# Kernel tuning notes

Measured on AMD Instinct MI355X. Metric: run time of the kernel, lower is better.

## Reference

```python
import jax, jax.numpy as jnp
import numpy as np
import math

D_MODEL = 1024
NHEAD = 16
HEAD_DIM = D_MODEL // NHEAD
ROPE_BASE = 10000.0


def _rope(x):
    # x: [B, H, S, Dh]; rotate per the RoPE class (half-split variant)
    d = x.shape[-1]
    half = d // 2
    seq_len = x.shape[2]
    theta = 1.0 / (ROPE_BASE ** (jnp.arange(0, d, 2, dtype=jnp.float32) / d))  # [d/2]
    ang = jnp.arange(seq_len, dtype=jnp.float32)[:, None] * theta[None, :]      # [S, d/2]
    ang2 = jnp.concatenate([ang, ang], axis=-1)                                 # [S, d]
    cos_ = jnp.cos(ang2)[None, None, :, :]
    sin_ = jnp.sin(ang2)[None, None, :, :]
    neg_half = jnp.concatenate([-x[..., half:], x[..., :half]], axis=-1)
    return x * cos_ + neg_half * sin_


def setup_inputs() -> dict:
    key = jax.random.key(0)
    ks = jax.random.split(key, 10)
    B, S, D = 4, 2048, D_MODEL
    scale = 1.0 / math.sqrt(D)
    x = jax.random.normal(ks[0], (B, S, D), dtype=jnp.float32)
    Wq = jax.random.normal(ks[1], (D, D), dtype=jnp.float32) * scale
    bq = jnp.zeros((D,), dtype=jnp.float32)
    Wk = jax.random.normal(ks[2], (D, D), dtype=jnp.float32) * scale
    bk = jnp.zeros((D,), dtype=jnp.float32)
    Wv = jax.random.normal(ks[3], (D, D), dtype=jnp.float32) * scale
    bv = jnp.zeros((D,), dtype=jnp.float32)
    Wo = jax.random.normal(ks[4], (D, D), dtype=jnp.float32) * scale
    bo = jnp.zeros((D,), dtype=jnp.float32)
    # causal mask: mask==1 means masked (upper triangle)
    mask = jnp.triu(jnp.ones((S, S), dtype=jnp.int32), k=1)[None, None, :, :]
    return {"x": x, "Wq": Wq, "bq": bq, "Wk": Wk, "bk": bk,
            "Wv": Wv, "bv": bv, "Wo": Wo, "bo": bo, "mask": mask}


def reference(x, Wq, bq, Wk, bk, Wv, bv, Wo, bo, mask):
    B, S, D = x.shape
    H, Dh = NHEAD, HEAD_DIM

    def proj(W, b):
        y = jnp.einsum('bsd,ed->bse', x, W) + b  # torch Linear: x @ W.T + b
        return y.reshape(B, S, H, Dh).transpose(0, 2, 1, 3)  # [B,H,S,Dh]

    q = _rope(proj(Wq, bq))
    k = _rope(proj(Wk, bk))
    v = proj(Wv, bv)

    a = jnp.einsum('bhqd,bhkd->bhqk', q, k) / math.sqrt(Dh)  # [B,H,S,S]
    a = jnp.where(mask == 1, jnp.float32(-1e9), a)
    a = jax.nn.softmax(a, axis=-1)
    out = jnp.einsum('bhqk,bhkd->bhqd', a, v)                 # [B,H,S,Dh]
    out = out.transpose(0, 2, 1, 3).reshape(B, S, D)
    return jnp.einsum('bsd,ed->bse', out, Wo) + bo
```

## Files before the change

### kernel.cpp

```cpp
#include <hip/hip_runtime.h>
#include <stdint.h>

typedef unsigned short u16;
typedef __bf16 bf16x8 __attribute__((ext_vector_type(8)));
typedef __bf16 bf16x2 __attribute__((ext_vector_type(2)));
typedef float f32x4 __attribute__((ext_vector_type(4)));
typedef float f32x16 __attribute__((ext_vector_type(16)));

#define SEQ    2048
#define NHEAD  16
#define DH     64
#define DMODEL 1024
#define NBH    64

__device__ __forceinline__ u16 cvt1(float f){
  union { __bf16 h; u16 u; } c; c.h = (__bf16)f; return c.u;
}
__device__ __forceinline__ uint32_t cvt2(float a, float b){
  union { bf16x2 v; uint32_t u; } c; c.v = bf16x2{(__bf16)a, (__bf16)b}; return c.u;
}
__device__ __forceinline__ int swz(int row){ return (((row&7)^((row>>3)&7))<<4); }

#if __has_builtin(__builtin_amdgcn_exp2f)
__device__ __forceinline__ float EXP2(float x){ return __builtin_amdgcn_exp2f(x); }
#else
__device__ __forceinline__ float EXP2(float x){ return exp2f(x); }
#endif
__device__ __forceinline__ float max3f(float a, float b, float c){
  float r; asm("v_max3_f32 %0, %1, %2, %3" : "=v"(r) : "v"(a), "v"(b), "v"(c));
  return r;
}

typedef const __attribute__((address_space(1))) uint32_t* gas_t;
typedef __attribute__((address_space(3))) uint32_t* las_t;
__device__ __forceinline__ void async16(const void* g, void* l){
  __builtin_amdgcn_global_load_lds((gas_t)g, (las_t)l, 16, 0, 0);
}

__device__ __forceinline__ void vstore8(char* dst, uint2 a0, uint2 a1,
                                        uint2 b0, uint2 b1, int dc, int vpos){
  uint32_t pk[8];
  pk[0] = __builtin_amdgcn_perm(b0.x, a0.x, 0x05040100u);
  pk[1] = __builtin_amdgcn_perm(b0.x, a0.x, 0x07060302u);
  pk[2] = __builtin_amdgcn_perm(b0.y, a0.y, 0x05040100u);
  pk[3] = __builtin_amdgcn_perm(b0.y, a0.y, 0x07060302u);
  pk[4] = __builtin_amdgcn_perm(b1.x, a1.x, 0x05040100u);
  pk[5] = __builtin_amdgcn_perm(b1.x, a1.x, 0x07060302u);
  pk[6] = __builtin_amdgcn_perm(b1.y, a1.y, 0x05040100u);
  pk[7] = __builtin_amdgcn_perm(b1.y, a1.y, 0x07060302u);
#pragma unroll
  for (int e=0;e<8;e++){
    const int row = dc*8 + e;
    *(uint32_t*)(dst + ((row*128 + vpos*2) ^ swz(row))) = pk[e];
  }
}

__global__ void prep(const float* __restrict__ x,  const float* __restrict__ Wq,
                     const float* __restrict__ Wk, const float* __restrict__ Wv,
                     const float* __restrict__ Wo,
                     u16* __restrict__ xb, u16* __restrict__ wqkv,
                     u16* __restrict__ wob, float* __restrict__ tab)
{
  const int bid = blockIdx.x, tid = threadIdx.x;
  if (bid < 6144){
    const float* src; u16* dst; int lb;
    if      (bid < 4096){ src = x;  dst = xb;              lb = bid; }
    else if (bid < 4608){ src = Wq; dst = wqkv;            lb = bid-4096; }
    else if (bid < 5120){ src = Wk; dst = wqkv + 1048576;  lb = bid-4608; }
    else if (bid < 5632){ src = Wv; dst = wqkv + 2097152;  lb = bid-5120; }
    else                { src = Wo; dst = wob;             lb = bid-5632; }
    const size_t off = (size_t)lb*2048 + tid*8;
    float4 a = *(const float4*)(src+off);
    float4 b = *(const float4*)(src+off+4);
    bf16x8 o = { (__bf16)a.x,(__bf16)a.y,(__bf16)a.z,(__bf16)a.w,
                 (__bf16)b.x,(__bf16)b.y,(__bf16)b.z,(__bf16)b.w };
    *(bf16x8*)(dst+off) = o;
  } else {
    const int t = (bid-6144)*256 + tid;
    const int s = t >> 5, j = t & 31;
    double freq = exp(-(double)(2*j)/64.0*log(10000.0));
    double ang = (double)s*freq;
    tab[s*64 + 2*j]     = (float)cos(ang);
    tab[s*64 + 2*j + 1] = (float)sin(ang);
  }
}

template<int MODE>
__global__ __launch_bounds__(256, 2)
void gemm_bt(const u16* __restrict__ A, const u16* __restrict__ W,
             const float* __restrict__ b0, const float* __restrict__ b1,
             const float* __restrict__ b2, float* __restrict__ fout,
             u16* __restrict__ dq, u16* __restrict__ dk, u16* __restrict__ dv,
             const float* __restrict__ tab)
{
  __shared__ u16 Ab[2][128*32];
  __shared__ u16 Bb[2][128*32];
  const int tid = threadIdx.x;
  const int lane = tid & 63;
  const int w = tid >> 6, wr = w >> 1, wc = w & 1;
  const int m0 = blockIdx.y * 128;
  const int n0 = blockIdx.x * 128;
  const int c0 = lane & 15, g = lane >> 4;

  f32x4 acc[4][4] = {};

  const int sr = tid >> 2;
  const int sc16 = tid & 3;
  const int stoff = sr*64 + sc16*16;
  const int gsw = (sc16*16) ^ ((sr & 3) << 4);
  const char* ga = (const char*)A + (size_t)(m0 + sr)*DMODEL*2 + gsw;
  const char* gb = (const char*)W + (size_t)(n0 + sr)*DMODEL*2 + gsw;

#define STAGE_G(buf, kk) do{ \
    async16(ga + 2*(kk),              (char*)Ab[buf] + stoff); \
    async16(ga + 2*(kk) + 128*DMODEL, (char*)Ab[buf] + stoff + 4096); \
    async16(gb + 2*(kk),              (char*)Bb[buf] + stoff); \
    async16(gb + 2*(kk) + 128*DMODEL, (char*)Bb[buf] + stoff + 4096); \
  }while(0)

#define COMPUTE_G(buf) do{ \
    bf16x8 afr[4], bfr[4]; \
    _Pragma("unroll") \
    for (int i=0;i<4;i++){ \
      const int row = wr*64 + i*16 + c0; \
      afr[i] = *(const bf16x8*)((const char*)Ab[buf] + row*64 + ((g*16) ^ ((row&3)<<4))); \
    } \
    _Pragma("unroll") \
    for (int j=0;j<4;j++){ \
      const int row = wc*64 + j*16 + c0; \
      bfr[j] = *(const bf16x8*)((const char*)Bb[buf] + row*64 + ((g*16) ^ ((row&3)<<4))); \
    } \
    __builtin_amdgcn_s_setprio(1); \
    _Pragma("unroll") \
    for (int i=0;i<4;i++) \
      _Pragma("unroll") \
      for (int j=0;j<4;j++) \
        acc[i][j] = __builtin_amdgcn_mfma_f32_16x16x32_bf16(afr[i], bfr[j], acc[i][j], 0,0,0); \
    __builtin_amdgcn_s_setprio(0); \
  }while(0)

  STAGE_G(0, 0);
#pragma unroll 2
  for (int k0 = 0; k0 < DMODEL - 32; k0 += 32) {
    const int cur = (k0 >> 5) & 1;
    STAGE_G(cur ^ 1, k0 + 32);
    asm volatile("s_waitcnt vmcnt(4)" ::: "memory");
    __builtin_amdgcn_s_barrier();
    __builtin_amdgcn_sched_barrier(0);
    COMPUTE_G(cur);
    __builtin_amdgcn_s_barrier();
    __builtin_amdgcn_sched_barrier(0);
  }
  asm volatile("s_waitcnt vmcnt(0)" ::: "memory");
  __builtin_amdgcn_s_barrier();
  __builtin_amdgcn_sched_barrier(0);
  COMPUTE_G(1);
#undef STAGE_G
#undef COMPUTE_G

  const int nbase = n0 + wc*64;
  const int t = n0 >> 10;
  const float* bias = (MODE==1) ? b0 : (t==0) ? b0 : (t==1) ? b1 : b2;
  float bv4[4];
#pragma unroll
  for (int j=0;j<4;j++) bv4[j] = bias[(nbase & 1023) + j*16 + c0];

  if (MODE == 0) {
    u16* dst = (t==0) ? dq : (t==1) ? dk : dv;
    const float qs = (t==0) ? 0.18033688011f : 1.0f;
    const int h = (nbase >> 6) & (NHEAD-1);
#pragma unroll
    for (int i=0;i<4;i++){
      const int mbase = m0 + wr*64 + i*16 + g*4;
#pragma unroll
      for (int r=0;r<4;r++){
        const int mm = mbase + r;
        const int bb = mm >> 11, s = mm & (SEQ-1);
        const size_t rowbase = (((size_t)(bb*NHEAD + h))*SEQ + s)*DH;
        if (t < 2) {
#pragma unroll
          for (int j2=0;j2<2;j2++){
            const int dh = j2*16 + c0;
            const float xl = acc[i][j2][r]   + bv4[j2];
            const float xh = acc[i][j2+2][r] + bv4[j2+2];
            const float2 cs = *(const float2*)(tab + (size_t)s*64 + dh*2);
            dst[rowbase + dh]      = cvt1((xl*cs.x - xh*cs.y)*qs);
            dst[rowbase + dh + 32] = cvt1((xh*cs.x + xl*cs.y)*qs);
          }
        } else {
#pragma unroll
          for (int j=0;j<4;j++)
            dst[rowbase + j*16 + c0] = cvt1(acc[i][j][r] + bv4[j]);
        }
      }
    }
  } else {
#pragma unroll
    for (int i=0;i<4;i++){
      const int mbase = m0 + wr*64 + i*16 + g*4;
#pragma unroll
      for (int j=0;j<4;j++){
#pragma unroll
        for (int r=0;r<4;r++)
          fout[(size_t)(mbase + r) * DMODEL + nbase + j*16 + c0] = acc[i][j][r] + bv4[j];
      }
    }
  }
}

__global__ __launch_bounds__(256, 2)
void attn_fwd(const u16* __restrict__ Q, const u16* __restrict__ K,
              const u16* __restrict__ V, u16* __restrict__ O)
{
  __shared__ u16 Kb[2][64*64];
  __shared__ u16 Vt[2][64*64];
  const int bh = blockIdx.x;
  const int pair = blockIdx.y;
  const int tid = threadIdx.x, lane = tid & 63, w = tid >> 6;
  const int c31 = lane & 31, hi = lane >> 5;
  const size_t hb = (size_t)bh * SEQ * DH;
  const int b = bh >> 4, h = bh & 15;

  const int boff1 = tid*16;
  const int ksw1  = boff1 ^ swz(boff1 >> 7);
  const int boff2 = boff1 + 4096;
  const int ksw2  = boff2 ^ swz(boff2 >> 7);
  const int rp = tid >> 3, dc = tid & 7;
  const int kv0 = 2*rp;
  const int vpos = (kv0 & 0x33) | ((kv0 & 4) << 1) | ((kv0 & 8) >> 1);

#pragma unroll 1
  for (int half = 0; half < 2; half++){
    const int qt = half ? (15 - pair) : pair;
    const int qrow_base = qt*128 + w*32;
    const int jt_last  = 2*qt + 1;
    const int jt_end_w = 2*qt + (w>>1);
    const int q = qrow_base + c31;

    bf16x8 qf[4];
#pragma unroll
    for (int kc=0;kc<4;kc++)
      qf[kc] = *(const bf16x8*)(Q + hb + (size_t)q*DH + kc*16 + hi*8);

    f32x16 oacc0 = {}, oacc1 = {};
    float mrun = -3.0e38f, lrun = 0.f;

    {
      const char* gk = (const char*)(K + hb);
      async16(gk + ksw1, (char*)Kb[0] + boff1);
      async16(gk + ksw2, (char*)Kb[0] + boff2);
      const u16* gv = V + hb;
      uint2 a0 = *(const uint2*)(gv + (kv0  )*DH + dc*8);
      uint2 a1 = *(const uint2*)(gv + (kv0  )*DH + dc*8 + 4);
      uint2 b0 = *(const uint2*)(gv + (kv0+1)*DH + dc*8);
      uint2 b1 = *(const uint2*)(gv + (kv0+1)*DH + dc*8 + 4);
      vstore8((char*)Vt[0], a0, a1, b0, b1, dc, vpos);
    }
    __syncthreads();

    uint2 pa0, pa1, pb0, pb1;
    for (int jt = 0; jt <= jt_last; jt++){
      const int cur = jt & 1, nxt = cur ^ 1;
      const bool pre = (jt < jt_last);
      if (pre){
        const char* gk = (const char*)(K + hb + (size_t)(jt+1)*64*DH);
        async16(gk + ksw1, (char*)Kb[nxt] + boff1);
        async16(gk + ksw2, (char*)Kb[nxt] + boff2);
        const u16* gv = V + hb + (size_t)(jt+1)*64*DH;
        pa0 = *(const uint2*)(gv + (kv0  )*DH + dc*8);
        pa1 = *(const uint2*)(gv + (kv0  )*DH + dc*8 + 4);
        pb0 = *(const uint2*)(gv + (kv0+1)*DH + dc*8);
        pb1 = *(const uint2*)(gv + (kv0+1)*DH + dc*8 + 4);
      }

      if (jt <= jt_end_w){
        f32x16 sT[2] = {};
#pragma unroll
        for (int kc=0;kc<4;kc++){
          const int col = (kc*16 + hi*8)*2;
          const int r0 = c31, r1 = 32 + c31;
          const bf16x8 kf0 = *(const bf16x8*)((const char*)Kb[cur] + ((r0*128 + col) ^ swz(r0)));
          const bf16x8 kf1 = *(const bf16x8*)((const char*)Kb[cur] + ((r1*128 + col) ^ swz(r1)));
          __builtin_amdgcn_s_setprio(1);
          sT[0] = __builtin_amdgcn_mfma_f32_32x32x16_bf16(kf0, qf[kc], sT[0], 0,0,0);
          sT[1] = __builtin_amdgcn_mfma_f32_32x32x16_bf16(kf1, qf[kc], sT[1], 0,0,0);
          __builtin_amdgcn_s_setprio(0);
        }
        if (jt == jt_end_w){
#pragma unroll
          for (int kvb=0;kvb<2;kvb++)
#pragma unroll
            for (int r=0;r<16;r++){
              const int kv = jt*64 + kvb*32 + (r&3) + 8*(r>>2) + 4*hi;
              sT[kvb][r] = (kv <= q) ? sT[kvb][r] : -3.0e38f;
            }
        }
        float mx0 = -3.0e38f, mx1 = -3.0e38f;
#pragma unroll
        for (int r=0;r<16;r+=2){
          mx0 = max3f(mx0, sT[0][r], sT[0][r+1]);
          mx1 = max3f(mx1, sT[1][r], sT[1][r+1]);
        }
        float mx = fmaxf(mx0, mx1);
        mx = fmaxf(mx, __shfl_xor(mx, 32));
        const bool grow = __any(mx > mrun + 8.0f);
        float corr = 1.0f;
        if (grow){
          const float mnew = fmaxf(mrun, mx);
          corr = EXP2(mrun - mnew);
          mrun = mnew;
        }
        float ls[4] = {0.f, 0.f, 0.f, 0.f};
#pragma unroll
        for (int kvb=0;kvb<2;kvb++)
#pragma unroll
          for (int r=0;r<16;r++){
            const float p = EXP2(sT[kvb][r] - mrun);
            sT[kvb][r] = p;
            ls[r & 3] += p;
          }
        float lsum = (ls[0] + ls[1]) + (ls[2] + ls[3]);
        lsum += __shfl_xor(lsum, 32);
        lrun = lrun*corr + lsum;
        if (grow){
#pragma unroll
          for (int r=0;r<16;r++){ oacc0[r] *= corr; oacc1[r] *= corr; }
        }
#pragma unroll
        for (int kvb=0;kvb<2;kvb++)
#pragma unroll
          for (int s=0;s<2;s++){
            union { bf16x8 v; uint32_t d[4]; } pa;
#pragma unroll
            for (int j=0;j<4;j++)
              pa.d[j] = cvt2(sT[kvb][s*8+2*j], sT[kvb][s*8+2*j+1]);
            const int col = (kvb*32 + s*16 + hi*8)*2;
            const int r0 = c31, r1 = 32 + c31;
            const bf16x8 vf0 = *(const bf16x8*)((const char*)Vt[cur] + ((r0*128 + col) ^ swz(r0)));
            const bf16x8 vf1 = *(const bf16x8*)((const char*)Vt[cur] + ((r1*128 + col) ^ swz(r1)));
            __builtin_amdgcn_s_setprio(1);
            oacc0 = __builtin_amdgcn_mfma_f32_32x32x16_bf16(vf0, pa.v, oacc0, 0,0,0);
            oacc1 = __builtin_amdgcn_mfma_f32_32x32x16_bf16(vf1, pa.v, oacc1, 0,0,0);
            __builtin_amdgcn_s_setprio(0);
          }
      }

      if (pre) vstore8((char*)Vt[nxt], pa0, pa1, pb0, pb1, dc, vpos);
      __syncthreads();
    }

    {
      const float inv = 1.0f / lrun;
      u16* orow = O + ((size_t)b*SEQ + q)*DMODEL + h*DH;
#pragma unroll
      for (int r2=0;r2<8;r2++){
        const int dh0 = 2*(r2&1) + 8*(r2>>1) + 4*hi;
        *(uint32_t*)(orow + dh0)      = cvt2(oacc0[2*r2]*inv, oacc0[2*r2+1]*inv);
        *(uint32_t*)(orow + 32 + dh0) = cvt2(oacc1[2*r2]*inv, oacc1[2*r2+1]*inv);
      }
    }
  }
}

extern "C" void kernel_launch(void* const* d_in, const int* in_sizes, int n_in,
                              void* d_out, int out_size, void* d_ws, size_t ws_size,
                              hipStream_t stream)
{
  const float* x  = (const float*)d_in[0];
  const float* Wq = (const float*)d_in[1];
  const float* bq = (const float*)d_in[2];
  const float* Wk = (const float*)d_in[3];
  const float* bk = (const float*)d_in[4];
  const float* Wv = (const float*)d_in[5];
  const float* bv = (const float*)d_in[6];
  const float* Wo = (const float*)d_in[7];
  const float* bo = (const float*)d_in[8];

  const size_t MB = 1024*1024;
  char* ws = (char*)d_ws;
  u16*  xb   = (u16*)(ws);
  u16*  aw   = (u16*)(ws);
  u16*  vw   = (u16*)(ws + 16*MB);
  u16*  wqkv = (u16*)(ws + 32*MB);
  u16*  wob  = (u16*)(ws + 38*MB);
  float* tab = (float*)(ws + 41*MB);
  u16*  qw = (u16*)d_out;
  u16*  kw = (u16*)d_out + 8*MB;

  prep<<<dim3(6400), dim3(256), 0, stream>>>(x, Wq, Wk, Wv, Wo, xb, wqkv, wob, tab);

  gemm_bt<0><<<dim3(24, 64), dim3(256), 0, stream>>>(xb, wqkv, bq, bk, bv,
                                                     nullptr, qw, kw, vw, tab);

  attn_fwd<<<dim3(64, 8), dim3(256), 0, stream>>>(qw, kw, vw, aw);

  gemm_bt<1><<<dim3(8, 64), dim3(256), 0, stream>>>(aw, wob, bo, nullptr, nullptr,
                                                    (float*)d_out, nullptr, nullptr, nullptr, nullptr);
}
```

Baseline: 172.2 us.

## Triple-buffer GEMM K-loop and remap block IDs for L2 tile locality

The GEMM's shared-memory staging goes from double to triple buffering, so global loads run two K-steps ahead of compute. The loop is manually unrolled by three, with a deeper vmcnt wait and an explicit two-step tail. The 2D grid becomes a 1D grid with a swizzled block-to-tile mapping that groups M tiles, aiming for better L2 reuse of A/W panels. The extra shared memory (48KB per block) may reduce occupancy relative to the launch_bounds target.

```diff
diff --git a/kernel.cpp b/kernel.cpp
--- a/kernel.cpp
+++ b/kernel.cpp
@@ -93,13 +93,16 @@
              u16* __restrict__ dq, u16* __restrict__ dk, u16* __restrict__ dv,
              const float* __restrict__ tab)
 {
-  __shared__ u16 Ab[2][128*32];
-  __shared__ u16 Bb[2][128*32];
+  __shared__ u16 Ab[3][128*32];
+  __shared__ u16 Bb[3][128*32];
   const int tid = threadIdx.x;
   const int lane = tid & 63;
   const int w = tid >> 6, wr = w >> 1, wc = w & 1;
-  const int m0 = blockIdx.y * 128;
-  const int n0 = blockIdx.x * 128;
+  const int id = blockIdx.x;
+  const int bx = id >> 6;
+  const int by = ((id & 7) << 3) | ((id >> 3) & 7);
+  const int m0 = by * 128;
+  const int n0 = bx * 128;
   const int c0 = lane & 15, g = lane >> 4;
 
   f32x4 acc[4][4] = {};
@@ -139,24 +142,38 @@
     __builtin_amdgcn_s_setprio(0); \
   }while(0)
 
+#define PHASE_G(itv, sb, cb) do{ \
+    STAGE_G(sb, ((itv)+2)*32); \
+    asm volatile("s_waitcnt vmcnt(8)" ::: "memory"); \
+    __builtin_amdgcn_s_barrier(); \
+    __builtin_amdgcn_sched_barrier(0); \
+    COMPUTE_G(cb); \
+    __builtin_amdgcn_s_barrier(); \
+    __builtin_amdgcn_sched_barrier(0); \
+  }while(0)
+
   STAGE_G(0, 0);
-#pragma unroll 2
-  for (int k0 = 0; k0 < DMODEL - 32; k0 += 32) {
-    const int cur = (k0 >> 5) & 1;
-    STAGE_G(cur ^ 1, k0 + 32);
-    asm volatile("s_waitcnt vmcnt(4)" ::: "memory");
-    __builtin_amdgcn_s_barrier();
-    __builtin_amdgcn_sched_barrier(0);
-    COMPUTE_G(cur);
-    __builtin_amdgcn_s_barrier();
-    __builtin_amdgcn_sched_barrier(0);
+  STAGE_G(1, 32);
+#pragma unroll 1
+  for (int j3 = 0; j3 < 10; ++j3) {
+    const int it = 3*j3;
+    PHASE_G(it,   2, 0);
+    PHASE_G(it+1, 0, 1);
+    PHASE_G(it+2, 1, 2);
   }
+  asm volatile("s_waitcnt vmcnt(4)" ::: "memory");
+  __builtin_amdgcn_s_barrier();
+  __builtin_amdgcn_sched_barrier(0);
+  COMPUTE_G(0);
+  __builtin_amdgcn_s_barrier();
+  __builtin_amdgcn_sched_barrier(0);
   asm volatile("s_waitcnt vmcnt(0)" ::: "memory");
   __builtin_amdgcn_s_barrier();
   __builtin_amdgcn_sched_barrier(0);
   COMPUTE_G(1);
 #undef STAGE_G
 #undef COMPUTE_G
+#undef PHASE_G
 
   const int nbase = n0 + wc*64;
   const int t = n0 >> 10;
@@ -389,11 +406,11 @@
 
   prep<<<dim3(6400), dim3(256), 0, stream>>>(x, Wq, Wk, Wv, Wo, xb, wqkv, wob, tab);
 
-  gemm_bt<0><<<dim3(24, 64), dim3(256), 0, stream>>>(xb, wqkv, bq, bk, bv,
-                                                     nullptr, qw, kw, vw, tab);
+  gemm_bt<0><<<dim3(1536), dim3(256), 0, stream>>>(xb, wqkv, bq, bk, bv,
+                                                   nullptr, qw, kw, vw, tab);
 
   attn_fwd<<<dim3(64, 8), dim3(256), 0, stream>>>(qw, kw, vw, aw);
 
-  gemm_bt<1><<<dim3(8, 64), dim3(256), 0, stream>>>(aw, wob, bo, nullptr, nullptr,
-                                                    (float*)d_out, nullptr, nullptr, nullptr, nullptr);
-}
+  gemm_bt<1><<<dim3(512), dim3(256), 0, stream>>>(aw, wob, bo, nullptr, nullptr,
+                                                  (float*)d_out, nullptr, nullptr, nullptr, nullptr);
+}
```

New measurement: 166.3 us. 1.04x faster.

## Deepen GEMM K-tile to 64 and remap blocks to a 1D swizzled grid

Applied to the files above, without the earlier changes.

The projection GEMMs now stage 64-wide K slices instead of 32, with an 8-way XOR shared-memory swizzle. This halves the number of barrier-separated iterations and doubles the MFMA work per sync. The launch grid becomes 1D, and the block ID is permuted so consecutive blocks share the same column tile while spreading across M, which should improve L2 reuse. Shared memory doubles to 64KB per block, which may limit occupancy under the launch bound of 2.

```diff
diff --git a/kernel.cpp b/kernel.cpp
--- a/kernel.cpp
+++ b/kernel.cpp
@@ -93,58 +93,63 @@
              u16* __restrict__ dq, u16* __restrict__ dk, u16* __restrict__ dv,
              const float* __restrict__ tab)
 {
-  __shared__ u16 Ab[2][128*32];
-  __shared__ u16 Bb[2][128*32];
+  __shared__ u16 Ab[2][128*64];
+  __shared__ u16 Bb[2][128*64];
   const int tid = threadIdx.x;
   const int lane = tid & 63;
   const int w = tid >> 6, wr = w >> 1, wc = w & 1;
-  const int m0 = blockIdx.y * 128;
-  const int n0 = blockIdx.x * 128;
+  const int id = blockIdx.x;
+  const int bx = id >> 6;
+  const int by = ((id & 7) << 3) | ((id >> 3) & 7);
+  const int m0 = by * 128;
+  const int n0 = bx * 128;
   const int c0 = lane & 15, g = lane >> 4;
 
   f32x4 acc[4][4] = {};
 
-  const int sr = tid >> 2;
-  const int sc16 = tid & 3;
-  const int stoff = sr*64 + sc16*16;
-  const int gsw = (sc16*16) ^ ((sr & 3) << 4);
-  const char* ga = (const char*)A + (size_t)(m0 + sr)*DMODEL*2 + gsw;
-  const char* gb = (const char*)W + (size_t)(n0 + sr)*DMODEL*2 + gsw;
-
-#define STAGE_G(buf, kk) do{ \
-    async16(ga + 2*(kk),              (char*)Ab[buf] + stoff); \
-    async16(ga + 2*(kk) + 128*DMODEL, (char*)Ab[buf] + stoff + 4096); \
-    async16(gb + 2*(kk),              (char*)Bb[buf] + stoff); \
-    async16(gb + 2*(kk) + 128*DMODEL, (char*)Bb[buf] + stoff + 4096); \
+  const int srow = tid >> 3;
+  const int gcol = (((tid & 7) ^ (srow & 7)) << 4);
+  const char* ga = (const char*)A + (size_t)(m0 + srow)*2048 + gcol;
+  const char* gb = (const char*)W + (size_t)(n0 + srow)*2048 + gcol;
+  const int ldst = tid*16;
+
+#define STAGE_G(buf, kbyte) do{ \
+    _Pragma("unroll") \
+    for (int k=0;k<4;k++){ \
+      async16(ga + (kbyte) + k*32*2048, (char*)Ab[buf] + k*4096 + ldst); \
+      async16(gb + (kbyte) + k*32*2048, (char*)Bb[buf] + k*4096 + ldst); \
+    } \
   }while(0)
 
 #define COMPUTE_G(buf) do{ \
-    bf16x8 afr[4], bfr[4]; \
+    bf16x8 afr[2][4], bfr[2][4]; \
     _Pragma("unroll") \
-    for (int i=0;i<4;i++){ \
-      const int row = wr*64 + i*16 + c0; \
-      afr[i] = *(const bf16x8*)((const char*)Ab[buf] + row*64 + ((g*16) ^ ((row&3)<<4))); \
-    } \
-    _Pragma("unroll") \
-    for (int j=0;j<4;j++){ \
-      const int row = wc*64 + j*16 + c0; \
-      bfr[j] = *(const bf16x8*)((const char*)Bb[buf] + row*64 + ((g*16) ^ ((row&3)<<4))); \
+    for (int kk=0;kk<2;kk++){ \
+      _Pragma("unroll") \
+      for (int i=0;i<4;i++){ \
+        const int ra = wr*64 + i*16 + c0; \
+        afr[kk][i] = *(const bf16x8*)((const char*)Ab[buf] + ra*128 + ((((kk*4+g) ^ (ra&7))) << 4)); \
+        const int rb = wc*64 + i*16 + c0; \
+        bfr[kk][i] = *(const bf16x8*)((const char*)Bb[buf] + rb*128 + ((((kk*4+g) ^ (rb&7))) << 4)); \
+      } \
     } \
     __builtin_amdgcn_s_setprio(1); \
     _Pragma("unroll") \
-    for (int i=0;i<4;i++) \
+    for (int kk=0;kk<2;kk++) \
       _Pragma("unroll") \
-      for (int j=0;j<4;j++) \
-        acc[i][j] = __builtin_amdgcn_mfma_f32_16x16x32_bf16(afr[i], bfr[j], acc[i][j], 0,0,0); \
+      for (int i=0;i<4;i++) \
+        _Pragma("unroll") \
+        for (int j=0;j<4;j++) \
+          acc[i][j] = __builtin_amdgcn_mfma_f32_16x16x32_bf16(afr[kk][i], bfr[kk][j], acc[i][j], 0,0,0); \
     __builtin_amdgcn_s_setprio(0); \
   }while(0)
 
   STAGE_G(0, 0);
-#pragma unroll 2
-  for (int k0 = 0; k0 < DMODEL - 32; k0 += 32) {
-    const int cur = (k0 >> 5) & 1;
-    STAGE_G(cur ^ 1, k0 + 32);
-    asm volatile("s_waitcnt vmcnt(4)" ::: "memory");
+#pragma unroll 1
+  for (int it = 0; it < 15; ++it) {
+    const int cur = it & 1;
+    STAGE_G(cur ^ 1, (it+1)*128);
+    asm volatile("s_waitcnt vmcnt(8)" ::: "memory");
     __builtin_amdgcn_s_barrier();
     __builtin_amdgcn_sched_barrier(0);
     COMPUTE_G(cur);
@@ -389,11 +394,11 @@
 
   prep<<<dim3(6400), dim3(256), 0, stream>>>(x, Wq, Wk, Wv, Wo, xb, wqkv, wob, tab);
 
-  gemm_bt<0><<<dim3(24, 64), dim3(256), 0, stream>>>(xb, wqkv, bq, bk, bv,
-                                                     nullptr, qw, kw, vw, tab);
+  gemm_bt<0><<<dim3(1536), dim3(256), 0, stream>>>(xb, wqkv, bq, bk, bv,
+                                                   nullptr, qw, kw, vw, tab);
 
   attn_fwd<<<dim3(64, 8), dim3(256), 0, stream>>>(qw, kw, vw, aw);
 
-  gemm_bt<1><<<dim3(8, 64), dim3(256), 0, stream>>>(aw, wob, bo, nullptr, nullptr,
-                                                    (float*)d_out, nullptr, nullptr, nullptr, nullptr);
-}
+  gemm_bt<1><<<dim3(512), dim3(256), 0, stream>>>(aw, wob, bo, nullptr, nullptr,
+                                                  (float*)d_out, nullptr, nullptr, nullptr, nullptr);
+}
```

New measurement: 162.9 us. 1.06x faster.
